# Optimization experiments

Measured on AMD Instinct MI355X. Metric: run time of the kernel, lower is better.

The kernel has to match this reference:

```python
import jax, jax.numpy as jnp
import numpy as np
from jax import lax

EPS = 1e-5
C4 = 192   # embed_dim // 4
ED = 768   # embed_dim


def _conv(x, w, stride, pad):
    return lax.conv_general_dilated(x, w, (stride, stride), pad,
                                    dimension_numbers=('NCHW', 'OIHW', 'NCHW'))


def _bn(x, g, b, m, v):
    # inference-mode batchnorm over channel dim (NCHW)
    inv = g * lax.rsqrt(v + EPS)
    return x * inv[None, :, None, None] + (b - m * inv)[None, :, None, None]


def _gelu(x):
    return jax.nn.gelu(x, approximate=False)  # torch nn.GELU default = exact erf


def _region(x, w, g, b, m, v, grid):
    # x: (B,C,H,W); w: (G,C,C,3,3); bn params: (G,C); G = gh*gw
    B, C, H, W = x.shape
    gh, gw = grid
    th, tw = H // gh, W // gw
    tiles = x.reshape(B, C, gh, th, gw, tw).transpose(2, 4, 0, 1, 3, 5)
    tiles = tiles.reshape(gh * gw, B, C, th, tw)

    def per_tile(t, wi, gi, bi, mi, vi):
        y = _gelu(_bn(_conv(t, wi, 1, 'SAME'), gi, bi, mi, vi))
        return y + t  # residual

    out = jax.vmap(per_tile)(tiles, w, g, b, m, v)  # (G,B,C,th,tw)
    out = out.reshape(gh, gw, B, C, th, tw).transpose(2, 3, 0, 4, 1, 5)
    return out.reshape(B, C, H, W)


def _bn_params(key, c):
    k1, k2, k3, k4 = jax.random.split(key, 4)
    return (1.0 + 0.1 * jax.random.normal(k1, (c,)),
            0.1 * jax.random.normal(k2, (c,)),
            0.1 * jax.random.normal(k3, (c,)),
            jax.random.uniform(k4, (c,), minval=0.5, maxval=1.5))


def setup_inputs() -> dict:
    key = jax.random.key(0)
    ks = jax.random.split(key, 12)
    x = jax.random.normal(ks[0], (64, 3, 224, 224), dtype=jnp.float32)
    conv1_w = 0.02 * jax.random.normal(ks[1], (C4, 3, 4, 4))
    bn1_g, bn1_b, bn1_m, bn1_v = _bn_params(ks[2], C4)
    r1_w = 0.02 * jax.random.normal(ks[3], (64, C4, C4, 3, 3))
    r1_g, r1_b, r1_m, r1_v = _bn_params(ks[4], C4)
    r1_g, r1_b, r1_m, r1_v = (jnp.tile(p[None], (64, 1)) * (1.0 + 0.01 * jax.random.normal(jax.random.fold_in(ks[4], i), (64, C4))) for i, p in enumerate((r1_g, r1_b, r1_m, r1_v)))
    conv2_w = 0.02 * jax.random.normal(ks[5], (C4, C4, 2, 2))
    bn2_g, bn2_b, bn2_m, bn2_v = _bn_params(ks[6], C4)
    r2_w = 0.02 * jax.random.normal(ks[7], (16, C4, C4, 3, 3))
    r2_g, r2_b, r2_m, r2_v = _bn_params(ks[8], C4)
    r2_g, r2_b, r2_m, r2_v = (jnp.tile(p[None], (16, 1)) * (1.0 + 0.01 * jax.random.normal(jax.random.fold_in(ks[8], i), (16, C4))) for i, p in enumerate((r2_g, r2_b, r2_m, r2_v)))
    conv3_w = 0.02 * jax.random.normal(ks[9], (ED, C4, 2, 2))
    bn3_g, bn3_b, bn3_m, bn3_v = _bn_params(ks[10], ED)
    return dict(x=x, conv1_w=conv1_w, bn1_g=bn1_g, bn1_b=bn1_b, bn1_m=bn1_m, bn1_v=bn1_v,
                r1_w=r1_w, r1_g=r1_g, r1_b=r1_b, r1_m=r1_m, r1_v=r1_v,
                conv2_w=conv2_w, bn2_g=bn2_g, bn2_b=bn2_b, bn2_m=bn2_m, bn2_v=bn2_v,
                r2_w=r2_w, r2_g=r2_g, r2_b=r2_b, r2_m=r2_m, r2_v=r2_v,
                conv3_w=conv3_w, bn3_g=bn3_g, bn3_b=bn3_b, bn3_m=bn3_m, bn3_v=bn3_v)


def reference(x, conv1_w, bn1_g, bn1_b, bn1_m, bn1_v,
              r1_w, r1_g, r1_b, r1_m, r1_v,
              conv2_w, bn2_g, bn2_b, bn2_m, bn2_v,
              r2_w, r2_g, r2_b, r2_m, r2_v,
              conv3_w, bn3_g, bn3_b, bn3_m, bn3_v):
    h = _gelu(_bn(_conv(x, conv1_w, 4, 'VALID'), bn1_g, bn1_b, bn1_m, bn1_v))   # (B,192,56,56)
    h = _region(h, r1_w, r1_g, r1_b, r1_m, r1_v, (8, 8))
    h = _gelu(_bn(_conv(h, conv2_w, 2, 'VALID'), bn2_g, bn2_b, bn2_m, bn2_v))   # (B,192,28,28)
    h = _region(h, r2_w, r2_g, r2_b, r2_m, r2_v, (4, 4))
    h = _bn(_conv(h, conv3_w, 2, 'VALID'), bn3_g, bn3_b, bn3_m, bn3_v)          # (B,768,14,14)
    B = h.shape[0]
    return h.reshape(B, ED, -1).transpose(0, 2, 1)                               # (B,196,768)
```

## Files before the change

### kernel.cpp

```cpp
#include <hip/hip_runtime.h>
#include <hip/hip_bf16.h>
#include <math.h>

#define EPSBN 1e-5f

typedef short short8 __attribute__((ext_vector_type(8)));
typedef short short4v __attribute__((ext_vector_type(4)));
typedef float floatx4 __attribute__((ext_vector_type(4)));

__device__ __forceinline__ float gelu_f(float x) {
    return 0.5f * x * (1.0f + erff(x * 0.70710678118654752f));
}

__device__ __forceinline__ unsigned short f2bf(float f) {
    union { float f; unsigned int u; } c; c.f = f;
    unsigned int u = c.u;
    unsigned int r = (u + 0x7FFFu + ((u >> 16) & 1u)) >> 16;
    return (unsigned short)r;
}

__device__ __forceinline__ float bf2f(unsigned short h) {
    union { unsigned int u; float f; } c; c.u = ((unsigned int)h) << 16;
    return c.f;
}

__device__ __forceinline__ void gl16(const unsigned short* g, unsigned short* l) {
    __builtin_amdgcn_global_load_lds(
        (const __attribute__((address_space(1))) unsigned int*)g,
        (__attribute__((address_space(3))) unsigned int*)l, 16, 0, 0);
}

__global__ void wprep_bf16_k(const float* __restrict__ w, unsigned short* __restrict__ wb,
                             long total) {
    for (long i = (long)blockIdx.x * blockDim.x + threadIdx.x; i < total;
         i += (long)gridDim.x * blockDim.x) {
        int ic = (int)(i % 192);
        long t1 = i / 192;
        int oc = (int)(t1 % 192);
        long g = t1 / 192;
        const float* src = w + (size_t)i * 9;
        int s = ic >> 5, q = (ic >> 3) & 3, e = ic & 7;
        int bnd = oc / 48, ocl = oc % 48;
        size_t ob = (size_t)g * 331776 + (size_t)s * 6144 + bnd * 1536 + q * 384 + ocl * 8 + e;
        #pragma unroll
        for (int t = 0; t < 9; t++)
            wb[ob + (size_t)t * 36864] = f2bf(src[t]);
    }
}

__global__ void wprep_tap_k(const float* __restrict__ w, unsigned short* __restrict__ wb,
                            int OC) {
    long total = (long)4 * OC * 192;
    for (long o = (long)blockIdx.x * blockDim.x + threadIdx.x; o < total;
         o += (long)gridDim.x * blockDim.x) {
        int ic = (int)(o % 192); long t0 = o / 192;
        int oc = (int)(t0 % OC); int t = (int)(t0 / OC);
        wb[o] = f2bf(w[((size_t)oc * 192 + ic) * 4 + t]);
    }
}

__global__ void wprep_wt1_k(const float* __restrict__ w, float* __restrict__ wt) {
    int o = blockIdx.x * 256 + threadIdx.x;
    if (o < 9216) {
        int oc = o % 192, k = o / 192;
        wt[o] = w[oc * 48 + k];
    }
}

__global__ __launch_bounds__(192) void conv1_k(
        const float* __restrict__ x, const float* __restrict__ wt1,
        const float* __restrict__ bg, const float* __restrict__ bb,
        const float* __restrict__ bm, const float* __restrict__ bv,
        unsigned short* __restrict__ h1c) {
    __shared__ float xs[3][4][224];
    int b = blockIdx.x / 56, oy = blockIdx.x % 56;
    int tid = threadIdx.x;
    for (int i = tid; i < 2688; i += 192) {
        int col = i % 224, r = (i / 224) % 4, c = i / 896;
        xs[c][r][col] = x[(((size_t)b * 3 + c) * 224 + 4 * oy + r) * 224 + col];
    }
    float w[48];
    #pragma unroll
    for (int k = 0; k < 48; k++) w[k] = wt1[k * 192 + tid];
    float inv = bg[tid] * rsqrtf(bv[tid] + EPSBN);
    float bet = bb[tid] - bm[tid] * inv;
    __syncthreads();
    for (int ox = 0; ox < 56; ox++) {
        float a = 0.f;
        #pragma unroll
        for (int c = 0; c < 3; c++) {
            #pragma unroll
            for (int ky = 0; ky < 4; ky++) {
                float4 v = *(const float4*)&xs[c][ky][4 * ox];
                const float* wk = &w[(c * 4 + ky) * 4];
                a += v.x * wk[0] + v.y * wk[1] + v.z * wk[2] + v.w * wk[3];
            }
        }
        h1c[(((size_t)b * 56 + oy) * 56 + ox) * 192 + tid] = f2bf(gelu_f(a * inv + bet));
    }
}

#define RSTC 200
#define ZCELL 98
#define AW0 19800
#define AW1 25944
template<int INF32>
__global__ __launch_bounds__(256, 2) void region_stage_k(
        const void* __restrict__ inbuf, void* __restrict__ outbuf,
        const unsigned short* __restrict__ wb,
        const float* __restrict__ pg, const float* __restrict__ pb,
        const float* __restrict__ pm, const float* __restrict__ pv,
        int gw, int W, int bofs) {
    __shared__ unsigned short lds[32088];
    const int raw = blockIdx.x + bofs;
    const int g = (raw & 7) + 8 * (raw >> 8);
    const int bp = (raw >> 3) & 31;
    const int b0 = bp * 2;
    const int gy = g / gw, gx = g % gw;
    const int Y0 = gy * 7, X0 = gx * 7;
    const int tid = threadIdx.x;
    const int lane = tid & 63;
    const int wid = tid >> 6;
    const int quad = lane >> 4;
    const int l15 = lane & 15;

    const size_t tsz = (size_t)W * W * 192;
    const size_t slab0 = (size_t)b0 * tsz;
    const unsigned short* wbg = wb + (size_t)g * 331776;

    {
        const unsigned short* s0 = wbg + wid * 1536 + lane * 8;
        unsigned short* d0 = &lds[AW0 + wid * 1536];
        gl16(s0, d0); gl16(s0 + 512, d0 + 512); gl16(s0 + 1024, d0 + 1024);
        const unsigned short* s1 = wbg + 6144 + wid * 1536 + lane * 8;
        unsigned short* d1 = &lds[AW1 + wid * 1536];
        gl16(s1, d1); gl16(s1 + 512, d1 + 512); gl16(s1 + 1024, d1 + 1024);
    }

    if (tid < 24) *(short8*)&lds[ZCELL * RSTC + tid * 8] = (short8)0;
    for (int i = tid; i < 2352; i += 256) {
        int tI = i / 1176, rem = i % 1176, p = rem / 24, ch = rem % 24;
        int y = p / 7, xx = p % 7;
        size_t poff = slab0 + (size_t)tI * tsz + ((size_t)(Y0 + y) * W + (X0 + xx)) * 192 + ch * 8;
        short8 v;
        if (INF32) {
            const float* s4 = (const float*)inbuf + poff;
            float4 a = *(const float4*)s4;
            float4 b2 = *(const float4*)(s4 + 4);
            v[0] = (short)f2bf(a.x);  v[1] = (short)f2bf(a.y);
            v[2] = (short)f2bf(a.z);  v[3] = (short)f2bf(a.w);
            v[4] = (short)f2bf(b2.x); v[5] = (short)f2bf(b2.y);
            v[6] = (short)f2bf(b2.z); v[7] = (short)f2bf(b2.w);
        } else {
            v = *(const short8*)((const unsigned short*)inbuf + poff);
        }
        *(short8*)&lds[(tI * 49 + p) * RSTC + ch * 8] = v;
    }
    __syncthreads();

    int pyv[4], pxv[4];
    #pragma unroll
    for (int f = 0; f < 4; f++) {
        int p = f * 16 + l15; if (p > 48) p = 48;
        pyv[f] = p / 7; pxv[f] = p % 7;
    }
    int wbo[3];
    #pragma unroll
    for (int nt = 0; nt < 3; nt++)
        wbo[nt] = wid * 1536 + quad * 384 + (nt * 16 + l15) * 8;

    floatx4 acc[8][3];
    #pragma unroll
    for (int m = 0; m < 8; m++)
        #pragma unroll
        for (int nt = 0; nt < 3; nt++) acc[m][nt] = (floatx4)0.f;

    int ca[8];
#define SET_CA(TT) { const int ky = (TT) / 3, kx = (TT) % 3; \
    _Pragma("unroll") for (int f = 0; f < 4; f++) { \
        int iy = pyv[f] + ky - 1, ix = pxv[f] + kx - 1; \
        bool ok = ((unsigned)iy < 7u) && ((unsigned)ix < 7u); \
        int c0 = ok ? (iy * 7 + ix) : ZCELL; \
        ca[f] = c0 * RSTC + quad * 8; \
        ca[4 + f] = (ok ? (c0 + 49) : ZCELL) * RSTC + quad * 8; } }

#define COMPUTE(WBASE, SL) { short8 wfv[3], pfv[8]; \
    _Pragma("unroll") for (int nt = 0; nt < 3; nt++) \
        wfv[nt] = *(const short8*)&lds[(WBASE) + wbo[nt]]; \
    _Pragma("unroll") for (int m = 0; m < 8; m++) \
        pfv[m] = *(const short8*)&lds[ca[m] + (SL) * 32]; \
    _Pragma("unroll") for (int m = 0; m < 8; m++) \
        _Pragma("unroll") for (int nt = 0; nt < 3; nt++) \
            acc[m][nt] = __builtin_amdgcn_mfma_f32_16x16x32_bf16(pfv[m], wfv[nt], acc[m][nt], 0, 0, 0); }

#define STAGE(WBASE, N) { asm volatile("" ::: "memory"); \
    const unsigned short* sg = wbg + (size_t)(N) * 6144 + wid * 1536 + lane * 8; \
    unsigned short* dl = &lds[(WBASE) + wid * 1536]; \
    gl16(sg, dl); gl16(sg + 512, dl + 512); gl16(sg + 1024, dl + 1024); }

    SET_CA(0);
    int sn = 0, tn = 0;
    #pragma unroll 1
    for (int k = 0; k < 26; k++) {
        asm volatile("s_waitcnt vmcnt(3)" ::: "memory");
        COMPUTE(AW0, sn);
        STAGE(AW0, 2 * k + 2);
        asm volatile("s_waitcnt vmcnt(3)" ::: "memory");
        COMPUTE(AW1, sn + 1);
        STAGE(AW1, 2 * k + 3);
        sn += 2;
        if (sn == 6) { sn = 0; tn++; SET_CA(tn); }
    }
    asm volatile("s_waitcnt vmcnt(0)" ::: "memory");
    COMPUTE(AW0, 4);
    COMPUTE(AW1, 5);

#undef SET_CA
#undef COMPUTE
#undef STAGE

    #pragma unroll
    for (int nt = 0; nt < 3; nt++) {
        int oc = wid * 48 + nt * 16 + l15;
        float inv = pg[g * 192 + oc] * rsqrtf(pv[g * 192 + oc] + EPSBN);
        float bet = pb[g * 192 + oc] - pm[g * 192 + oc] * inv;
        #pragma unroll
        for (int m = 0; m < 8; m++) {
            const int tI = m >> 2;
            const int f = m & 3;
            const size_t tslab = slab0 + (size_t)tI * tsz;
            unsigned short* outb = (unsigned short*)outbuf + tslab;
            const float* resf = (const float*)inbuf + tslab;
            #pragma unroll
            for (int r = 0; r < 4; r++) {
                int p = f * 16 + quad * 4 + r;
                if (p < 49) {
                    int y = p / 7, xx = p % 7;
                    size_t pix = (size_t)(Y0 + y) * W + (X0 + xx);
                    float res = INF32 ? resf[pix * 192 + oc]
                                      : bf2f(lds[(tI * 49 + p) * RSTC + oc]);
                    outb[pix * 192 + oc] = f2bf(gelu_f(acc[m][nt][r] * inv + bet) + res);
                }
            }
        }
    }
}

__global__ __launch_bounds__(256) void conv2_mfma_k(
        const unsigned short* __restrict__ h1c, const unsigned short* __restrict__ wb,
        const float* __restrict__ bg, const float* __restrict__ bb,
        const float* __restrict__ bm, const float* __restrict__ bv,
        float* __restrict__ h2c) {
    __shared__ unsigned short lds[2 * 56 * 40];
    const int b = blockIdx.x / 14;
    const int oy0 = (blockIdx.x % 14) * 2;
    const int tid = threadIdx.x;
    const int lane = tid & 63;
    const int wid = tid >> 6;
    const int quad = lane >> 4;
    const int l15 = lane & 15;

    floatx4 acc[4][3];
    #pragma unroll
    for (int mt = 0; mt < 4; mt++)
        #pragma unroll
        for (int nt = 0; nt < 3; nt++) acc[mt][nt] = (floatx4)0.f;

    for (int ky = 0; ky < 2; ky++) {
        for (int c = 0; c < 6; c++) {
            short8 wpre[2][3];
            #pragma unroll
            for (int kx = 0; kx < 2; kx++) {
                const int t = ky * 2 + kx;
                #pragma unroll
                for (int nt = 0; nt < 3; nt++) {
                    int oc = wid * 48 + nt * 16 + l15;
                    wpre[kx][nt] = *(const short8*)(wb + ((size_t)(t * 192 + oc)) * 192 + c * 32 + quad * 8);
                }
            }
            __syncthreads();
            for (int i = tid; i < 896; i += 256) {
                int icq = i & 7, kx = (i >> 3) & 1, p = i >> 4;
                int oy = oy0 + p / 28, ox = p % 28;
                int iy = 2 * oy + ky, ix = 2 * ox + kx;
                const unsigned short* src =
                    h1c + (((size_t)b * 56 + iy) * 56 + ix) * 192 + c * 32 + icq * 4;
                *(short4v*)(&lds[kx * 2240 + p * 40 + icq * 4]) = *(const short4v*)src;
            }
            __syncthreads();
            #pragma unroll
            for (int kx = 0; kx < 2; kx++) {
                #pragma unroll
                for (int mt = 0; mt < 4; mt++) {
                    int p = mt * 16 + l15; if (p > 55) p = 55;
                    short8 ap = *(const short8*)(&lds[kx * 2240 + p * 40 + quad * 8]);
                    #pragma unroll
                    for (int nt = 0; nt < 3; nt++)
                        acc[mt][nt] = __builtin_amdgcn_mfma_f32_16x16x32_bf16(ap, wpre[kx][nt], acc[mt][nt], 0, 0, 0);
                }
            }
        }
    }
    #pragma unroll
    for (int nt = 0; nt < 3; nt++) {
        int oc = wid * 48 + nt * 16 + l15;
        float inv = bg[oc] * rsqrtf(bv[oc] + EPSBN);
        float bet = bb[oc] - bm[oc] * inv;
        #pragma unroll
        for (int mt = 0; mt < 4; mt++) {
            #pragma unroll
            for (int r = 0; r < 4; r++) {
                int p = mt * 16 + quad * 4 + r;
                if (p < 56) {
                    int oy = oy0 + p / 28, ox = p % 28;
                    h2c[(((size_t)b * 28 + oy) * 28 + ox) * 192 + oc] = gelu_f(acc[mt][nt][r] * inv + bet);
                }
            }
        }
    }
}

__global__ __launch_bounds__(256) void conv3_mfma_k(
        const unsigned short* __restrict__ h2b, const unsigned short* __restrict__ wb,
        const float* __restrict__ bg, const float* __restrict__ bb,
        const float* __restrict__ bm, const float* __restrict__ bv,
        float* __restrict__ out) {
    __shared__ unsigned short lds[2 * 28 * 40];
    const int bid = blockIdx.x;
    const int b = bid / 21;
    const int sy = (bid % 21) / 3;
    const int octile = bid % 3;
    const int tid = threadIdx.x;
    const int lane = tid & 63;
    const int wid = tid >> 6;
    const int quad = lane >> 4;
    const int l15 = lane & 15;

    floatx4 acc[2][4];
    #pragma unroll
    for (int mt = 0; mt < 2; mt++)
        #pragma unroll
        for (int nt = 0; nt < 4; nt++) acc[mt][nt] = (floatx4)0.f;

    for (int ky = 0; ky < 2; ky++) {
        for (int c = 0; c < 6; c++) {
            short8 wpre[2][4];
            #pragma unroll
            for (int kx = 0; kx < 2; kx++) {
                const int t = ky * 2 + kx;
                #pragma unroll
                for (int nt = 0; nt < 4; nt++) {
                    int oc = octile * 256 + wid * 64 + nt * 16 + l15;
                    wpre[kx][nt] = *(const short8*)(wb + ((size_t)(t * 768 + oc)) * 192 + c * 32 + quad * 8);
                }
            }
            __syncthreads();
            for (int i = tid; i < 448; i += 256) {
                int icq = i & 7, kx = (i >> 3) & 1, p = i >> 4;
                int oy = sy * 2 + p / 14, ox = p % 14;
                int iy = 2 * oy + ky, ix = 2 * ox + kx;
                const unsigned short* src =
                    h2b + (((size_t)b * 28 + iy) * 28 + ix) * 192 + c * 32 + icq * 4;
                *(short4v*)(&lds[kx * 1120 + p * 40 + icq * 4]) = *(const short4v*)src;
            }
            __syncthreads();
            #pragma unroll
            for (int kx = 0; kx < 2; kx++) {
                #pragma unroll
                for (int mt = 0; mt < 2; mt++) {
                    int p = mt * 16 + l15; if (p > 27) p = 27;
                    short8 ap = *(const short8*)(&lds[kx * 1120 + p * 40 + quad * 8]);
                    #pragma unroll
                    for (int nt = 0; nt < 4; nt++)
                        acc[mt][nt] = __builtin_amdgcn_mfma_f32_16x16x32_bf16(ap, wpre[kx][nt], acc[mt][nt], 0, 0, 0);
                }
            }
        }
    }
    #pragma unroll
    for (int nt = 0; nt < 4; nt++) {
        int oc = octile * 256 + wid * 64 + nt * 16 + l15;
        float inv = bg[oc] * rsqrtf(bv[oc] + EPSBN);
        float bet = bb[oc] - bm[oc] * inv;
        #pragma unroll
        for (int mt = 0; mt < 2; mt++) {
            #pragma unroll
            for (int r = 0; r < 4; r++) {
                int p = mt * 16 + quad * 4 + r;
                if (p < 28) {
                    int oy = sy * 2 + p / 14, ox = p % 14;
                    out[((size_t)b * 196 + oy * 14 + ox) * 768 + oc] = acc[mt][nt][r] * inv + bet;
                }
            }
        }
    }
}

extern "C" void kernel_launch(void* const* d_in, const int* in_sizes, int n_in,
                              void* d_out, int out_size, void* d_ws, size_t ws_size,
                              hipStream_t stream) {
    const float* x   = (const float*)d_in[0];
    const float* w1  = (const float*)d_in[1];
    const float* b1g = (const float*)d_in[2];
    const float* b1b = (const float*)d_in[3];
    const float* b1m = (const float*)d_in[4];
    const float* b1v = (const float*)d_in[5];
    const float* r1w = (const float*)d_in[6];
    const float* r1g = (const float*)d_in[7];
    const float* r1b = (const float*)d_in[8];
    const float* r1m = (const float*)d_in[9];
    const float* r1v = (const float*)d_in[10];
    const float* w2  = (const float*)d_in[11];
    const float* b2g = (const float*)d_in[12];
    const float* b2b = (const float*)d_in[13];
    const float* b2m = (const float*)d_in[14];
    const float* b2v = (const float*)d_in[15];
    const float* r2w = (const float*)d_in[16];
    const float* r2g = (const float*)d_in[17];
    const float* r2b = (const float*)d_in[18];
    const float* r2m = (const float*)d_in[19];
    const float* r2v = (const float*)d_in[20];
    const float* w3  = (const float*)d_in[21];
    const float* b3g = (const float*)d_in[22];
    const float* b3b = (const float*)d_in[23];
    const float* b3m = (const float*)d_in[24];
    const float* b3v = (const float*)d_in[25];
    float* out = (float*)d_out;

    char* ws = (char*)d_ws;
    unsigned short* h1c  = (unsigned short*)(ws + 0);
    float*          h2c  = (float*)         (ws + 77070336UL);
    unsigned short* h2b  = (unsigned short*)(ws + 115605504UL);
    unsigned short* wb1  = (unsigned short*)(ws + 134873088UL);
    unsigned short* wb2r = (unsigned short*)(ws + 177340416UL);
    float*          wt1  = (float*)         (ws + 187957248UL);
    unsigned short* wb2c = (unsigned short*)(ws + 187994112UL);
    unsigned short* wb3c = (unsigned short*)(ws + 188289024UL);

    wprep_bf16_k<<<2048, 256, 0, stream>>>(r1w, wb1, (long)64 * 36864);
    wprep_bf16_k<<<2048, 256, 0, stream>>>(r2w, wb2r, (long)16 * 36864);
    wprep_tap_k<<<576, 256, 0, stream>>>(w2, wb2c, 192);
    wprep_tap_k<<<2304, 256, 0, stream>>>(w3, wb3c, 768);
    wprep_wt1_k<<<36, 256, 0, stream>>>(w1, wt1);

    conv1_k<<<64 * 56, 192, 0, stream>>>(x, wt1, b1g, b1b, b1m, b1v, h1c);
    region_stage_k<0><<<1024, 256, 0, stream>>>(h1c, h1c, wb1, r1g, r1b, r1m, r1v, 8, 56, 0);
    region_stage_k<0><<<1024, 256, 0, stream>>>(h1c, h1c, wb1, r1g, r1b, r1m, r1v, 8, 56, 1024);
    conv2_mfma_k<<<64 * 14, 256, 0, stream>>>(h1c, wb2c, b2g, b2b, b2m, b2v, h2c);
    region_stage_k<1><<<512, 256, 0, stream>>>(h2c, h2b, wb2r, r2g, r2b, r2m, r2v, 4, 28, 0);
    conv3_mfma_k<<<64 * 21, 256, 0, stream>>>(h2b, wb3c, b3g, b3b, b3m, b3v, out);
}
```

Measured before the change: 864.3 us.

## Rewrite conv1 patch-embed as bf16 MFMA GEMM with padded K

Replaces the scalar FP32 conv1 kernel, where each thread computed one output channel over a row, with an MFMA-based GEMM. Each block handles two output rows (112 pixels), stages the 4x4x3 input patches as bf16 im2col in LDS with K padded from 48 to 64, and runs 16x16x32 bf16 MFMAs against bf16 weights prepacked by a new prep kernel. BN and GELU are applied on the accumulators. This trades FP32 input and weight precision for bf16 and writes the output with a strided scatter pattern.

```diff
diff --git a/kernel.cpp b/kernel.cpp
--- a/kernel.cpp
+++ b/kernel.cpp
@@ -59,44 +59,81 @@
     }
 }
 
-__global__ void wprep_wt1_k(const float* __restrict__ w, float* __restrict__ wt) {
+__global__ void wprep_wc1_k(const float* __restrict__ w, unsigned short* __restrict__ wb) {
     int o = blockIdx.x * 256 + threadIdx.x;
-    if (o < 9216) {
-        int oc = o % 192, k = o / 192;
-        wt[o] = w[oc * 48 + k];
-    }
-}
-
-__global__ __launch_bounds__(192) void conv1_k(
-        const float* __restrict__ x, const float* __restrict__ wt1,
+    if (o < 12288) {
+        int k = o & 63, oc = o >> 6;
+        wb[o] = (k < 48) ? f2bf(w[oc * 48 + k]) : (unsigned short)0;
+    }
+}
+
+__global__ __launch_bounds__(256) void conv1_mfma_k(
+        const float* __restrict__ x, const unsigned short* __restrict__ wb1c,
         const float* __restrict__ bg, const float* __restrict__ bb,
         const float* __restrict__ bm, const float* __restrict__ bv,
         unsigned short* __restrict__ h1c) {
-    __shared__ float xs[3][4][224];
-    int b = blockIdx.x / 56, oy = blockIdx.x % 56;
-    int tid = threadIdx.x;
-    for (int i = tid; i < 2688; i += 192) {
-        int col = i % 224, r = (i / 224) % 4, c = i / 896;
-        xs[c][r][col] = x[(((size_t)b * 3 + c) * 224 + 4 * oy + r) * 224 + col];
-    }
-    float w[48];
-    #pragma unroll
-    for (int k = 0; k < 48; k++) w[k] = wt1[k * 192 + tid];
-    float inv = bg[tid] * rsqrtf(bv[tid] + EPSBN);
-    float bet = bb[tid] - bm[tid] * inv;
+    __shared__ unsigned short lds[112 * 72];
+    const int b = blockIdx.x / 28, oyp = blockIdx.x % 28;
+    const int tid = threadIdx.x;
+    const int lane = tid & 63;
+    const int wid = tid >> 6;
+    const int quad = lane >> 4;
+    const int l15 = lane & 15;
+
+    for (int i = tid; i < 1344; i += 256) {
+        int p = i / 12, j = i % 12, c = j >> 2, r = j & 3;
+        int oy = 2 * oyp + p / 56, ox = p % 56;
+        float4 v = *(const float4*)&x[(((size_t)b * 3 + c) * 224 + 4 * oy + r) * 224 + 4 * ox];
+        short4v s;
+        s[0] = (short)f2bf(v.x); s[1] = (short)f2bf(v.y);
+        s[2] = (short)f2bf(v.z); s[3] = (short)f2bf(v.w);
+        *(short4v*)&lds[p * 72 + c * 16 + r * 4] = s;
+    }
+    for (int i = tid; i < 224; i += 256) {
+        int p = i >> 1, h = i & 1;
+        *(short8*)&lds[p * 72 + 48 + h * 8] = (short8)0;
+    }
     __syncthreads();
-    for (int ox = 0; ox < 56; ox++) {
-        float a = 0.f;
-        #pragma unroll
-        for (int c = 0; c < 3; c++) {
-            #pragma unroll
-            for (int ky = 0; ky < 4; ky++) {
-                float4 v = *(const float4*)&xs[c][ky][4 * ox];
-                const float* wk = &w[(c * 4 + ky) * 4];
-                a += v.x * wk[0] + v.y * wk[1] + v.z * wk[2] + v.w * wk[3];
-            }
-        }
-        h1c[(((size_t)b * 56 + oy) * 56 + ox) * 192 + tid] = f2bf(gelu_f(a * inv + bet));
+
+    short8 wf[2][3];
+    #pragma unroll
+    for (int st = 0; st < 2; st++)
+        #pragma unroll
+        for (int nt = 0; nt < 3; nt++) {
+            int oc = wid * 48 + nt * 16 + l15;
+            wf[st][nt] = *(const short8*)&wb1c[oc * 64 + st * 32 + quad * 8];
+        }
+
+    floatx4 acc[7][3];
+    #pragma unroll
+    for (int mt = 0; mt < 7; mt++)
+        #pragma unroll
+        for (int nt = 0; nt < 3; nt++) acc[mt][nt] = (floatx4)0.f;
+
+    #pragma unroll
+    for (int st = 0; st < 2; st++)
+        #pragma unroll
+        for (int mt = 0; mt < 7; mt++) {
+            short8 ap = *(const short8*)&lds[(mt * 16 + l15) * 72 + st * 32 + quad * 8];
+            #pragma unroll
+            for (int nt = 0; nt < 3; nt++)
+                acc[mt][nt] = __builtin_amdgcn_mfma_f32_16x16x32_bf16(ap, wf[st][nt], acc[mt][nt], 0, 0, 0);
+        }
+
+    #pragma unroll
+    for (int nt = 0; nt < 3; nt++) {
+        int oc = wid * 48 + nt * 16 + l15;
+        float inv = bg[oc] * rsqrtf(bv[oc] + EPSBN);
+        float bet = bb[oc] - bm[oc] * inv;
+        #pragma unroll
+        for (int mt = 0; mt < 7; mt++) {
+            #pragma unroll
+            for (int r = 0; r < 4; r++) {
+                int p = mt * 16 + quad * 4 + r;
+                int oy = 2 * oyp + p / 56, ox = p % 56;
+                h1c[(((size_t)b * 56 + oy) * 56 + ox) * 192 + oc] = f2bf(gelu_f(acc[mt][nt][r] * inv + bet));
+            }
+        }
     }
 }
 
@@ -433,7 +470,7 @@
     unsigned short* h2b  = (unsigned short*)(ws + 115605504UL);
     unsigned short* wb1  = (unsigned short*)(ws + 134873088UL);
     unsigned short* wb2r = (unsigned short*)(ws + 177340416UL);
-    float*          wt1  = (float*)         (ws + 187957248UL);
+    unsigned short* wb1c = (unsigned short*)(ws + 187957248UL);
     unsigned short* wb2c = (unsigned short*)(ws + 187994112UL);
     unsigned short* wb3c = (unsigned short*)(ws + 188289024UL);
 
@@ -441,9 +478,9 @@
     wprep_bf16_k<<<2048, 256, 0, stream>>>(r2w, wb2r, (long)16 * 36864);
     wprep_tap_k<<<576, 256, 0, stream>>>(w2, wb2c, 192);
     wprep_tap_k<<<2304, 256, 0, stream>>>(w3, wb3c, 768);
-    wprep_wt1_k<<<36, 256, 0, stream>>>(w1, wt1);
-
-    conv1_k<<<64 * 56, 192, 0, stream>>>(x, wt1, b1g, b1b, b1m, b1v, h1c);
+    wprep_wc1_k<<<48, 256, 0, stream>>>(w1, wb1c);
+
+    conv1_mfma_k<<<64 * 28, 256, 0, stream>>>(x, wb1c, b1g, b1b, b1m, b1v, h1c);
     region_stage_k<0><<<1024, 256, 0, stream>>>(h1c, h1c, wb1, r1g, r1b, r1m, r1v, 8, 56, 0);
     region_stage_k<0><<<1024, 256, 0, stream>>>(h1c, h1c, wb1, r1g, r1b, r1m, r1v, 8, 56, 1024);
     conv2_mfma_k<<<64 * 14, 256, 0, stream>>>(h1c, wb2c, b2g, b2b, b2m, b2v, h2c);
```

After: 697.4 us. 1.24x faster.
